# Kernel tuning notes

Hardware: AMD Instinct MI355X
Metric: run time of the kernel (lower is better)

Reference implementation:

```python
import jax, jax.numpy as jnp
import numpy as np

B, C, H, W = 4, 32, 512, 1024  # input feature map
HO, WO = 512, 1024             # output grid


def setup_inputs() -> dict:
    key = jax.random.key(0)
    k1, k2 = jax.random.split(key)
    x = jax.random.normal(k1, (B, C, H, W), dtype=jnp.float32)
    # real-valued (x, y) output coordinates for every input pixel, in-bounds
    scale = jnp.asarray([WO - 1, HO - 1], dtype=jnp.float32)
    sample_map = jax.random.uniform(k2, (H, W, 2), dtype=jnp.float32) * scale
    return {"x": x, "sample_map": sample_map, "out_h": HO, "out_w": WO}


def reference(x, sample_map, out_h, out_w):
    """Bilinear splat: scatter each input pixel x[:,:,i,j] into the output
    at real-valued location sample_map[i,j] = (x_coord, y_coord)."""
    b, c, h, w = x.shape
    n = h * w
    coords = sample_map.reshape(n, 2)
    cx, cy = coords[:, 0], coords[:, 1]
    x0 = jnp.floor(cx)
    y0 = jnp.floor(cy)
    wx = cx - x0  # fractional offsets
    wy = cy - y0
    x0i = x0.astype(jnp.int32)
    y0i = y0.astype(jnp.int32)

    vals = x.reshape(b, c, n)
    out = jnp.zeros((b, c, out_h * out_w), dtype=x.dtype)
    # four bilinear corners: (xi, yi, weight)
    corners = (
        (x0i,     y0i,     (1.0 - wx) * (1.0 - wy)),
        (x0i + 1, y0i,     wx * (1.0 - wy)),
        (x0i,     y0i + 1, (1.0 - wx) * wy),
        (x0i + 1, y0i + 1, wx * wy),
    )
    for xi, yi, wgt in corners:
        valid = (xi >= 0) & (xi < out_w) & (yi >= 0) & (yi < out_h)
        idx = jnp.where(valid, yi * out_w + xi, 0)              # [n]
        wgt = jnp.where(valid, wgt, 0.0).astype(x.dtype)        # [n]
        out = out.at[:, :, idx].add(vals * wgt)
    return out.reshape(b, c, out_h, out_w)
```

## Files before the change

kernel.cpp:

```cpp
#include <hip/hip_runtime.h>

constexpr int Bc   = 4;
constexpr int Cc   = 32;
constexpr int Hc   = 512;
constexpr int Wc   = 1024;
constexpr int HOc  = 512;
constexpr int WOc  = 1024;
constexpr int NPIX  = Hc * Wc;
constexpr int PLANE = HOc * WOc;
constexpr int BCn   = Bc * Cc;

constexpr int TH = 32, TW = 32;
constexpr int TILES_X = WOc / TW;
constexpr int TILES_Y = HOc / TH;
constexpr int NT = TILES_X * TILES_Y;
constexpr int G  = 8;
constexpr int CG = BCn / G;
constexpr int LDSW   = TW + 1;
constexpr int TCELLS = (TH + 1) * (TW + 1);
constexpr int NBIN   = TCELLS + 1;
constexpr int NMAX   = 1280;
constexpr int EMAX   = 4 * NMAX;

__device__ __forceinline__ int tile_of(float cx, float cy, int& x0, int& y0) {
    x0 = (int)floorf(cx);
    y0 = (int)floorf(cy);
    int tx = min(max(x0 >> 5, 0), TILES_X - 1);
    int ty = min(max(y0 >> 5, 0), TILES_Y - 1);
    return ty * TILES_X + tx;
}

__global__ __launch_bounds__(256) void hist_kernel(
    const float2* __restrict__ smap, int* __restrict__ count)
{
    __shared__ int h[NT];
    for (int i = threadIdx.x; i < NT; i += 256) h[i] = 0;
    __syncthreads();
    const int stride = gridDim.x * 256;
    for (int p = blockIdx.x * 256 + threadIdx.x; p < NPIX; p += stride) {
        float2 c = smap[p];
        int x0, y0;
        int t = tile_of(c.x, c.y, x0, y0);
        atomicAdd(&h[t], 1);
    }
    __syncthreads();
    for (int i = threadIdx.x; i < NT; i += 256)
        if (h[i]) atomicAdd(&count[i], h[i]);
}

__global__ __launch_bounds__(512) void scan_kernel(
    const int* __restrict__ count, int* __restrict__ off)
{
    __shared__ int s[NT];
    int tid = threadIdx.x;
    s[tid] = count[tid];
    __syncthreads();
    for (int d = 1; d < NT; d <<= 1) {
        int v = (tid >= d) ? s[tid - d] : 0;
        __syncthreads();
        s[tid] += v;
        __syncthreads();
    }
    if (tid == 0) off[0] = 0;
    off[tid + 1] = s[tid];
}

__global__ __launch_bounds__(256) void scatter_pos_kernel(
    const float2* __restrict__ smap, const int* __restrict__ off,
    int* __restrict__ cursor, int* __restrict__ pos,
    float2* __restrict__ smap_g)
{
    __shared__ int h[NT];
    __shared__ int base[NT];
    const int tid = threadIdx.x;
    for (int i = tid; i < NT; i += 256) h[i] = 0;
    __syncthreads();
    const int p = blockIdx.x * 256 + tid;
    const float2 c = smap[p];
    int x0, y0;
    const int t = tile_of(c.x, c.y, x0, y0);
    atomicAdd(&h[t], 1);
    __syncthreads();
    for (int i = tid; i < NT; i += 256) {
        int cnt = h[i];
        base[i] = cnt ? atomicAdd(&cursor[i], cnt) : 0;
        h[i] = 0;
    }
    __syncthreads();
    const int r = atomicAdd(&h[t], 1);
    const int posi = off[t] + base[t] + r;
    pos[p] = posi;
    smap_g[posi] = c;
}

__global__ __launch_bounds__(256) void cellbuild_kernel(
    const float2* __restrict__ smap_g, const int* __restrict__ off,
    ushort* __restrict__ ent, float* __restrict__ entw,
    int* __restrict__ gcello)
{
    __shared__ unsigned cnt[NBIN];
    __shared__ unsigned coff[NBIN + 1];
    __shared__ unsigned psum[256];
    const int t   = blockIdx.x;
    const int tx0 = (t % TILES_X) * TW;
    const int ty0 = (t / TILES_X) * TH;
    const int lo  = off[t];
    const int n   = off[t + 1] - lo;
    const int nn  = min(n, NMAX);
    const int tid = threadIdx.x;

    for (int i = tid; i < NBIN; i += 256) cnt[i] = 0;
    __syncthreads();

    for (int i = tid; i < nn; i += 256) {
        float2 c = smap_g[lo + i];
        int x0 = (int)floorf(c.x), y0 = (int)floorf(c.y);
        int lx = x0 - tx0, ly = y0 - ty0;
        if ((unsigned)lx < (unsigned)TW && (unsigned)ly < (unsigned)TH) {
            int a = ly * LDSW + lx;
            atomicAdd(&cnt[a], 1u);
            atomicAdd(&cnt[a + 1], 1u);
            atomicAdd(&cnt[a + LDSW], 1u);
            atomicAdd(&cnt[a + LDSW + 1], 1u);
        } else {
            atomicAdd(&cnt[TCELLS], 1u);
        }
    }
    __syncthreads();

    constexpr int BPT = (NBIN + 255) / 256;
    unsigned loc[BPT];
    unsigned s = 0;
    for (int j = 0; j < BPT; ++j) {
        int b = tid * BPT + j;
        unsigned v = (b < NBIN) ? cnt[b] : 0u;
        loc[j] = s; s += v;
    }
    psum[tid] = s;
    __syncthreads();
    for (int d = 1; d < 256; d <<= 1) {
        unsigned v = (tid >= d) ? psum[tid - d] : 0u;
        __syncthreads();
        psum[tid] += v;
        __syncthreads();
    }
    unsigned base = (tid > 0) ? psum[tid - 1] : 0u;
    for (int j = 0; j < BPT; ++j) {
        int b = tid * BPT + j;
        if (b < NBIN) coff[b] = base + loc[j];
    }
    if (tid == 255) coff[NBIN] = psum[255];
    __syncthreads();

    for (int i = tid; i < NBIN; i += 256) cnt[i] = coff[i];
    for (int i = tid; i < NBIN + 1; i += 256)
        gcello[t * (NBIN + 1) + i] = (int)coff[i];
    __syncthreads();

    const int ebase = 4 * lo;
    for (int i = tid; i < nn; i += 256) {
        float2 c = smap_g[lo + i];
        float fx = floorf(c.x), fy = floorf(c.y);
        float wx = c.x - fx, wy = c.y - fy;
        int lx = (int)fx - tx0, ly = (int)fy - ty0;
        if ((unsigned)lx < (unsigned)TW && (unsigned)ly < (unsigned)TH) {
            int a = ly * LDSW + lx;
            float w00 = (1.f - wx) * (1.f - wy), w10 = wx * (1.f - wy);
            float w01 = (1.f - wx) * wy,         w11 = wx * wy;
            unsigned e;
            e = atomicAdd(&cnt[a], 1u);            ent[ebase + e] = (ushort)i; entw[ebase + e] = w00;
            e = atomicAdd(&cnt[a + 1], 1u);        ent[ebase + e] = (ushort)i; entw[ebase + e] = w10;
            e = atomicAdd(&cnt[a + LDSW], 1u);     ent[ebase + e] = (ushort)i; entw[ebase + e] = w01;
            e = atomicAdd(&cnt[a + LDSW + 1], 1u); ent[ebase + e] = (ushort)i; entw[ebase + e] = w11;
        } else {
            unsigned e = atomicAdd(&cnt[TCELLS], 1u);
            ent[ebase + e] = (ushort)i; entw[ebase + e] = 0.f;
        }
    }
}

__global__ __launch_bounds__(256) void gather_kernel(
    const float* __restrict__ x, const int* __restrict__ pos,
    float* __restrict__ xg, int cg0, int ncg)
{
    const int p = (blockIdx.x * 256 + threadIdx.x) * 4;
    const int4 d = *reinterpret_cast<const int4*>(pos + p);
    for (int g = 0; g < ncg; ++g) {
        const float* xp = x + (long)(cg0 + g) * G * NPIX + p;
        float4 r[8];
#pragma unroll
        for (int k = 0; k < 8; ++k)
            r[k] = *reinterpret_cast<const float4*>(xp + (long)k * NPIX);
        float* o0 = xg + ((long)g * NPIX + d.x) * 8;
        float* o1 = xg + ((long)g * NPIX + d.y) * 8;
        float* o2 = xg + ((long)g * NPIX + d.z) * 8;
        float* o3 = xg + ((long)g * NPIX + d.w) * 8;
        *reinterpret_cast<float4*>(o0)     = make_float4(r[0].x, r[1].x, r[2].x, r[3].x);
        *reinterpret_cast<float4*>(o0 + 4) = make_float4(r[4].x, r[5].x, r[6].x, r[7].x);
        *reinterpret_cast<float4*>(o1)     = make_float4(r[0].y, r[1].y, r[2].y, r[3].y);
        *reinterpret_cast<float4*>(o1 + 4) = make_float4(r[4].y, r[5].y, r[6].y, r[7].y);
        *reinterpret_cast<float4*>(o2)     = make_float4(r[0].z, r[1].z, r[2].z, r[3].z);
        *reinterpret_cast<float4*>(o2 + 4) = make_float4(r[4].z, r[5].z, r[6].z, r[7].z);
        *reinterpret_cast<float4*>(o3)     = make_float4(r[0].w, r[1].w, r[2].w, r[3].w);
        *reinterpret_cast<float4*>(o3 + 4) = make_float4(r[4].w, r[5].w, r[6].w, r[7].w);
    }
}

__global__ __launch_bounds__(512) void accum_kernel(
    const float*  __restrict__ xg,
    const float2* __restrict__ smap_g,
    const int*    __restrict__ off,
    const ushort* __restrict__ ent,
    const float*  __restrict__ entw,
    const int*    __restrict__ gcello,
    float*        __restrict__ out, int cg0)
{
    __shared__ float4   vals4[2 * NMAX];
    __shared__ float    wl[EMAX];
    __shared__ unsigned entl[EMAX / 2];
    __shared__ unsigned offl[NBIN + 1];
    const int t     = blockIdx.x;
    const int gslab = blockIdx.y;
    const int bc0   = (cg0 + gslab) * G;
    const int tx0 = (t % TILES_X) * TW;
    const int ty0 = (t / TILES_X) * TH;
    const int tid = threadIdx.x;
    const int lo = off[t], n = off[t + 1] - lo, nn = min(n, NMAX);
    const float* xs = xg + (long)gslab * NPIX * 8;

    const float4* vsrc = (const float4*)(xs + (long)lo * 8);
    for (int j = tid; j < nn * 2; j += 512) vals4[j] = vsrc[j];
    const unsigned* esrc = (const unsigned*)(ent + 4 * lo);
    for (int j = tid; j < nn * 2; j += 512) entl[j] = esrc[j];
    const float* wsrc = entw + 4 * lo;
    for (int j = tid; j < nn * 4; j += 512) wl[j] = wsrc[j];
    for (int j = tid; j < NBIN + 1; j += 512) offl[j] = (unsigned)gcello[t * (NBIN + 1) + j];
    __syncthreads();

    const ushort* entl16 = (const ushort*)entl;

    for (int c = tid; c < TCELLS; c += 512) {
        const unsigned e0 = offl[c], e1 = offl[c + 1];
        float a0 = 0, a1 = 0, a2 = 0, a3 = 0, a4 = 0, a5 = 0, a6 = 0, a7 = 0;
        for (unsigned e = e0; e < e1; ++e) {
            const int idx = entl16[e];
            const float w = wl[e];
            const float4 va = vals4[idx * 2];
            const float4 vb = vals4[idx * 2 + 1];
            a0 += va.x * w; a1 += va.y * w; a2 += va.z * w; a3 += va.w * w;
            a4 += vb.x * w; a5 += vb.y * w; a6 += vb.z * w; a7 += vb.w * w;
        }
        const int r = c / LDSW, cc = c - r * LDSW;
        const int gy = ty0 + r, gx = tx0 + cc;
        if (gy >= HOc || gx >= WOc) continue;
        const bool edge = (r == 0) | (cc == 0) | (r == TH) | (cc == TW);
        const long o = (long)gy * WOc + gx;
        const float av[8] = {a0, a1, a2, a3, a4, a5, a6, a7};
#pragma unroll
        for (int k = 0; k < 8; ++k) {
            float* op = out + (long)(bc0 + k) * PLANE + o;
            if (edge) { if (av[k] != 0.0f) unsafeAtomicAdd(op, av[k]); }
            else      { *op = av[k]; }
        }
    }
    __syncthreads();

    {
        const unsigned e0 = offl[TCELLS], e1 = offl[NBIN];
        for (unsigned e = e0 + tid; e < e1; e += 512) {
            const int idx = entl16[e];
            const float2 c2 = smap_g[lo + idx];
            const float fx = floorf(c2.x), fy = floorf(c2.y);
            const float wx = c2.x - fx, wy = c2.y - fy;
            const int x0 = (int)fx, y0 = (int)fy;
            const float4 va = vals4[idx * 2], vb = vals4[idx * 2 + 1];
            const float v[8] = {va.x, va.y, va.z, va.w, vb.x, vb.y, vb.z, vb.w};
            const float cw[4] = {(1.f - wx) * (1.f - wy), wx * (1.f - wy),
                                 (1.f - wx) * wy,         wx * wy};
            const int cxs[4] = {x0, x0 + 1, x0, x0 + 1};
            const int cys[4] = {y0, y0, y0 + 1, y0 + 1};
#pragma unroll
            for (int q = 0; q < 4; ++q) {
                if (cxs[q] < 0 || cxs[q] >= WOc || cys[q] < 0 || cys[q] >= HOc) continue;
                const long o = (long)cys[q] * WOc + cxs[q];
#pragma unroll
                for (int k = 0; k < 8; ++k)
                    unsafeAtomicAdd(out + (long)(bc0 + k) * PLANE + o, v[k] * cw[q]);
            }
        }
    }

    for (int i = NMAX + tid; i < n; i += 512) {
        const float2 c2 = smap_g[lo + i];
        const float fx = floorf(c2.x), fy = floorf(c2.y);
        const float wx = c2.x - fx, wy = c2.y - fy;
        const int x0 = (int)fx, y0 = (int)fy;
        const float4 va = *((const float4*)(xs + (long)(lo + i) * 8));
        const float4 vb = *((const float4*)(xs + (long)(lo + i) * 8) + 1);
        const float v[8] = {va.x, va.y, va.z, va.w, vb.x, vb.y, vb.z, vb.w};
        const float cw[4] = {(1.f - wx) * (1.f - wy), wx * (1.f - wy),
                             (1.f - wx) * wy,         wx * wy};
        const int cxs[4] = {x0, x0 + 1, x0, x0 + 1};
        const int cys[4] = {y0, y0, y0 + 1, y0 + 1};
#pragma unroll
        for (int q = 0; q < 4; ++q) {
            if (cxs[q] < 0 || cxs[q] >= WOc || cys[q] < 0 || cys[q] >= HOc) continue;
            const long o = (long)cys[q] * WOc + cxs[q];
#pragma unroll
            for (int k = 0; k < 8; ++k)
                unsafeAtomicAdd(out + (long)(bc0 + k) * PLANE + o, v[k] * cw[q]);
        }
    }
}

__global__ __launch_bounds__(256) void splat_kernel(
    const float* __restrict__ x, const float2* __restrict__ smap,
    float* __restrict__ out)
{
    const int p = blockIdx.x * blockDim.x + threadIdx.x;
    if (p >= NPIX) return;
    const float2 c = smap[p];
    const float x0f = floorf(c.x), y0f = floorf(c.y);
    const float wx = c.x - x0f, wy = c.y - y0f;
    const int x0 = (int)x0f, y0 = (int)y0f;
    const float w00 = (1.0f-wx)*(1.0f-wy), w10 = wx*(1.0f-wy);
    const float w01 = (1.0f-wx)*wy, w11 = wx*wy;
    const bool vx0 = (x0>=0)&(x0<WOc), vx1 = (x0+1>=0)&(x0+1<WOc);
    const bool vy0 = (y0>=0)&(y0<HOc), vy1 = (y0+1>=0)&(y0+1<HOc);
    const long base = (long)y0*WOc + x0;
    const int bc0 = blockIdx.y * 4;
#pragma unroll
    for (int k = 0; k < 4; ++k) {
        const int bc = bc0 + k;
        const float v = x[(long)bc*NPIX + p];
        float* o = out + (long)bc*PLANE;
        if (vx0 & vy0) unsafeAtomicAdd(o + base,          v*w00);
        if (vx1 & vy0) unsafeAtomicAdd(o + base + 1,      v*w10);
        if (vx0 & vy1) unsafeAtomicAdd(o + base + WOc,    v*w01);
        if (vx1 & vy1) unsafeAtomicAdd(o + base + WOc+1,  v*w11);
    }
}

extern "C" void kernel_launch(void* const* d_in, const int* in_sizes, int n_in,
                              void* d_out, int out_size, void* d_ws, size_t ws_size,
                              hipStream_t stream) {
    const float*  x    = (const float*)d_in[0];
    const float2* smap = (const float2*)d_in[1];
    float*        out  = (float*)d_out;

    hipMemsetAsync(d_out, 0, (size_t)out_size * sizeof(float), stream);

    const size_t ints = (size_t)NPIX + 3 * NT + 1 + (size_t)NT * (NBIN + 1);
    size_t ofs = (ints * sizeof(int) + 255) & ~(size_t)255;
    const size_t smapg_ofs = ofs;
    ofs += sizeof(float2) * (size_t)NPIX;
    ofs = (ofs + 255) & ~(size_t)255;
    const size_t ent_ofs = ofs;
    ofs += sizeof(ushort) * 4 * (size_t)NPIX;
    ofs = (ofs + 255) & ~(size_t)255;
    const size_t entw_ofs = ofs;
    ofs += sizeof(float) * 4 * (size_t)NPIX;
    ofs = (ofs + 255) & ~(size_t)255;
    const size_t xg_ofs = ofs;
    const size_t slab_bytes = (size_t)NPIX * G * sizeof(float);

    long slabs = 0;
    if (ws_size > xg_ofs) slabs = (long)((ws_size - xg_ofs) / slab_bytes);
    if (slabs > CG) slabs = CG;

    if (slabs < 1) {
        dim3 grid(NPIX / 256, BCn / 4);
        splat_kernel<<<grid, 256, 0, stream>>>(x, smap, out);
        return;
    }

    char* wsb      = (char*)d_ws;
    int*  pos      = (int*)wsb;
    int*  count    = pos + NPIX;
    int*  cursor   = count + NT;
    int*  off      = cursor + NT;
    int*  gcello   = off + NT + 1;
    float2* smap_g = (float2*)(wsb + smapg_ofs);
    ushort* ent    = (ushort*)(wsb + ent_ofs);
    float*  entw   = (float*)(wsb + entw_ofs);
    float*  xg     = (float*)(wsb + xg_ofs);

    hipMemsetAsync(count, 0, sizeof(int) * 2 * NT, stream);

    hist_kernel       <<<256, 256, 0, stream>>>(smap, count);
    scan_kernel       <<<1, 512, 0, stream>>>(count, off);
    scatter_pos_kernel<<<NPIX / 256, 256, 0, stream>>>(smap, off, cursor, pos, smap_g);
    cellbuild_kernel  <<<NT, 256, 0, stream>>>(smap_g, off, ent, entw, gcello);

    for (int cg0 = 0; cg0 < CG; cg0 += (int)slabs) {
        int ncg = CG - cg0;
        if (ncg > slabs) ncg = (int)slabs;
        gather_kernel<<<NPIX / 1024, 256, 0, stream>>>(x, pos, xg, cg0, ncg);
        dim3 grid2(NT, ncg);
        accum_kernel <<<grid2, 512, 0, stream>>>(xg, smap_g, off, ent, entw, gcello, out, cg0);
    }
}
```

Before: 1.981 ms.

## Drop LDS staging in accum kernel, read gathered values directly from global

The accumulation kernel no longer stages per-tile values, entry indices and weights into shared memory. It reads them straight from global memory, and the cache is expected to serve the reuse. The gathered layout widens to 16 channels per pixel, and each slab is split across two blocks of 8 channels. Both blocks of a pair touch the same pixel rows, which should improve cache locality. This removes the shared-memory footprint and the barriers, so occupancy can rise, but each entry now costs uncached-at-first global loads.

```diff
diff --git a/kernel.cpp b/kernel.cpp
--- a/kernel.cpp
+++ b/kernel.cpp
@@ -14,13 +14,12 @@
 constexpr int TILES_X = WOc / TW;
 constexpr int TILES_Y = HOc / TH;
 constexpr int NT = TILES_X * TILES_Y;
-constexpr int G  = 8;
-constexpr int CG = BCn / G;
+constexpr int CH16 = 16;
+constexpr int CG16 = BCn / CH16;
 constexpr int LDSW   = TW + 1;
 constexpr int TCELLS = (TH + 1) * (TW + 1);
 constexpr int NBIN   = TCELLS + 1;
 constexpr int NMAX   = 1280;
-constexpr int EMAX   = 4 * NMAX;
 
 __device__ __forceinline__ int tile_of(float cx, float cy, int& x0, int& y0) {
     x0 = (int)floorf(cx);
@@ -181,72 +180,61 @@
 
 __global__ __launch_bounds__(256) void gather_kernel(
     const float* __restrict__ x, const int* __restrict__ pos,
-    float* __restrict__ xg, int cg0, int ncg)
-{
-    const int p = (blockIdx.x * 256 + threadIdx.x) * 4;
-    const int4 d = *reinterpret_cast<const int4*>(pos + p);
-    for (int g = 0; g < ncg; ++g) {
-        const float* xp = x + (long)(cg0 + g) * G * NPIX + p;
-        float4 r[8];
-#pragma unroll
-        for (int k = 0; k < 8; ++k)
-            r[k] = *reinterpret_cast<const float4*>(xp + (long)k * NPIX);
-        float* o0 = xg + ((long)g * NPIX + d.x) * 8;
-        float* o1 = xg + ((long)g * NPIX + d.y) * 8;
-        float* o2 = xg + ((long)g * NPIX + d.z) * 8;
-        float* o3 = xg + ((long)g * NPIX + d.w) * 8;
-        *reinterpret_cast<float4*>(o0)     = make_float4(r[0].x, r[1].x, r[2].x, r[3].x);
-        *reinterpret_cast<float4*>(o0 + 4) = make_float4(r[4].x, r[5].x, r[6].x, r[7].x);
-        *reinterpret_cast<float4*>(o1)     = make_float4(r[0].y, r[1].y, r[2].y, r[3].y);
-        *reinterpret_cast<float4*>(o1 + 4) = make_float4(r[4].y, r[5].y, r[6].y, r[7].y);
-        *reinterpret_cast<float4*>(o2)     = make_float4(r[0].z, r[1].z, r[2].z, r[3].z);
-        *reinterpret_cast<float4*>(o2 + 4) = make_float4(r[4].z, r[5].z, r[6].z, r[7].z);
-        *reinterpret_cast<float4*>(o3)     = make_float4(r[0].w, r[1].w, r[2].w, r[3].w);
-        *reinterpret_cast<float4*>(o3 + 4) = make_float4(r[4].w, r[5].w, r[6].w, r[7].w);
-    }
-}
-
-__global__ __launch_bounds__(512) void accum_kernel(
+    float* __restrict__ xg, int cg016, int ncg16)
+{
+    const int p = (blockIdx.x * 256 + threadIdx.x) * 2;
+    const int2 d = *reinterpret_cast<const int2*>(pos + p);
+    for (int g = 0; g < ncg16; ++g) {
+        const float* xp = x + (long)(cg016 + g) * CH16 * NPIX + p;
+        float2 r[16];
+#pragma unroll
+        for (int k = 0; k < 16; ++k)
+            r[k] = *reinterpret_cast<const float2*>(xp + (long)k * NPIX);
+        float* o0 = xg + ((long)g * NPIX + d.x) * 16;
+        float* o1 = xg + ((long)g * NPIX + d.y) * 16;
+        *reinterpret_cast<float4*>(o0)      = make_float4(r[0].x,  r[1].x,  r[2].x,  r[3].x);
+        *reinterpret_cast<float4*>(o0 + 4)  = make_float4(r[4].x,  r[5].x,  r[6].x,  r[7].x);
+        *reinterpret_cast<float4*>(o0 + 8)  = make_float4(r[8].x,  r[9].x,  r[10].x, r[11].x);
+        *reinterpret_cast<float4*>(o0 + 12) = make_float4(r[12].x, r[13].x, r[14].x, r[15].x);
+        *reinterpret_cast<float4*>(o1)      = make_float4(r[0].y,  r[1].y,  r[2].y,  r[3].y);
+        *reinterpret_cast<float4*>(o1 + 4)  = make_float4(r[4].y,  r[5].y,  r[6].y,  r[7].y);
+        *reinterpret_cast<float4*>(o1 + 8)  = make_float4(r[8].y,  r[9].y,  r[10].y, r[11].y);
+        *reinterpret_cast<float4*>(o1 + 12) = make_float4(r[12].y, r[13].y, r[14].y, r[15].y);
+    }
+}
+
+__global__ __launch_bounds__(256) void accum_kernel(
     const float*  __restrict__ xg,
     const float2* __restrict__ smap_g,
     const int*    __restrict__ off,
     const ushort* __restrict__ ent,
     const float*  __restrict__ entw,
     const int*    __restrict__ gcello,
-    float*        __restrict__ out, int cg0)
-{
-    __shared__ float4   vals4[2 * NMAX];
-    __shared__ float    wl[EMAX];
-    __shared__ unsigned entl[EMAX / 2];
-    __shared__ unsigned offl[NBIN + 1];
-    const int t     = blockIdx.x;
-    const int gslab = blockIdx.y;
-    const int bc0   = (cg0 + gslab) * G;
+    float*        __restrict__ out, int cg016)
+{
+    const int t    = blockIdx.x;
+    const int yb   = blockIdx.y;
+    const int s16  = yb >> 1;
+    const int half = yb & 1;
+    const int bc0  = (cg016 + s16) * CH16 + half * 8;
     const int tx0 = (t % TILES_X) * TW;
     const int ty0 = (t / TILES_X) * TH;
     const int tid = threadIdx.x;
-    const int lo = off[t], n = off[t + 1] - lo, nn = min(n, NMAX);
-    const float* xs = xg + (long)gslab * NPIX * 8;
-
-    const float4* vsrc = (const float4*)(xs + (long)lo * 8);
-    for (int j = tid; j < nn * 2; j += 512) vals4[j] = vsrc[j];
-    const unsigned* esrc = (const unsigned*)(ent + 4 * lo);
-    for (int j = tid; j < nn * 2; j += 512) entl[j] = esrc[j];
-    const float* wsrc = entw + 4 * lo;
-    for (int j = tid; j < nn * 4; j += 512) wl[j] = wsrc[j];
-    for (int j = tid; j < NBIN + 1; j += 512) offl[j] = (unsigned)gcello[t * (NBIN + 1) + j];
-    __syncthreads();
-
-    const ushort* entl16 = (const ushort*)entl;
-
-    for (int c = tid; c < TCELLS; c += 512) {
-        const unsigned e0 = offl[c], e1 = offl[c + 1];
+    const int lo = off[t], n = off[t + 1] - lo;
+    const float*  xs = xg + ((long)s16 * NPIX + lo) * 16 + half * 8;
+    const ushort* ep = ent  + 4 * (long)lo;
+    const float*  wp = entw + 4 * (long)lo;
+    const int*    go = gcello + t * (NBIN + 1);
+
+    for (int c = tid; c < TCELLS; c += 256) {
+        const int e0 = go[c], e1 = go[c + 1];
         float a0 = 0, a1 = 0, a2 = 0, a3 = 0, a4 = 0, a5 = 0, a6 = 0, a7 = 0;
-        for (unsigned e = e0; e < e1; ++e) {
-            const int idx = entl16[e];
-            const float w = wl[e];
-            const float4 va = vals4[idx * 2];
-            const float4 vb = vals4[idx * 2 + 1];
+        for (int e = e0; e < e1; ++e) {
+            const int idx = ep[e];
+            const float w = wp[e];
+            const float* vp = xs + (long)idx * 16;
+            const float4 va = *reinterpret_cast<const float4*>(vp);
+            const float4 vb = *reinterpret_cast<const float4*>(vp + 4);
             a0 += va.x * w; a1 += va.y * w; a2 += va.z * w; a3 += va.w * w;
             a4 += vb.x * w; a5 += vb.y * w; a6 += vb.z * w; a7 += vb.w * w;
         }
@@ -263,17 +251,18 @@
             else      { *op = av[k]; }
         }
     }
-    __syncthreads();
 
     {
-        const unsigned e0 = offl[TCELLS], e1 = offl[NBIN];
-        for (unsigned e = e0 + tid; e < e1; e += 512) {
-            const int idx = entl16[e];
+        const int e0 = go[TCELLS], e1 = go[NBIN];
+        for (int e = e0 + tid; e < e1; e += 256) {
+            const int idx = ep[e];
             const float2 c2 = smap_g[lo + idx];
             const float fx = floorf(c2.x), fy = floorf(c2.y);
             const float wx = c2.x - fx, wy = c2.y - fy;
             const int x0 = (int)fx, y0 = (int)fy;
-            const float4 va = vals4[idx * 2], vb = vals4[idx * 2 + 1];
+            const float* vp = xs + (long)idx * 16;
+            const float4 va = *reinterpret_cast<const float4*>(vp);
+            const float4 vb = *reinterpret_cast<const float4*>(vp + 4);
             const float v[8] = {va.x, va.y, va.z, va.w, vb.x, vb.y, vb.z, vb.w};
             const float cw[4] = {(1.f - wx) * (1.f - wy), wx * (1.f - wy),
                                  (1.f - wx) * wy,         wx * wy};
@@ -290,13 +279,14 @@
         }
     }
 
-    for (int i = NMAX + tid; i < n; i += 512) {
+    for (int i = NMAX + tid; i < n; i += 256) {
         const float2 c2 = smap_g[lo + i];
         const float fx = floorf(c2.x), fy = floorf(c2.y);
         const float wx = c2.x - fx, wy = c2.y - fy;
         const int x0 = (int)fx, y0 = (int)fy;
-        const float4 va = *((const float4*)(xs + (long)(lo + i) * 8));
-        const float4 vb = *((const float4*)(xs + (long)(lo + i) * 8) + 1);
+        const float* vp = xs + (long)i * 16;
+        const float4 va = *reinterpret_cast<const float4*>(vp);
+        const float4 vb = *reinterpret_cast<const float4*>(vp + 4);
         const float v[8] = {va.x, va.y, va.z, va.w, vb.x, vb.y, vb.z, vb.w};
         const float cw[4] = {(1.f - wx) * (1.f - wy), wx * (1.f - wy),
                              (1.f - wx) * wy,         wx * wy};
@@ -362,11 +352,11 @@
     ofs += sizeof(float) * 4 * (size_t)NPIX;
     ofs = (ofs + 255) & ~(size_t)255;
     const size_t xg_ofs = ofs;
-    const size_t slab_bytes = (size_t)NPIX * G * sizeof(float);
+    const size_t slab_bytes = (size_t)NPIX * CH16 * sizeof(float);
 
     long slabs = 0;
     if (ws_size > xg_ofs) slabs = (long)((ws_size - xg_ofs) / slab_bytes);
-    if (slabs > CG) slabs = CG;
+    if (slabs > CG16) slabs = CG16;
 
     if (slabs < 1) {
         dim3 grid(NPIX / 256, BCn / 4);
@@ -392,11 +382,11 @@
     scatter_pos_kernel<<<NPIX / 256, 256, 0, stream>>>(smap, off, cursor, pos, smap_g);
     cellbuild_kernel  <<<NT, 256, 0, stream>>>(smap_g, off, ent, entw, gcello);
 
-    for (int cg0 = 0; cg0 < CG; cg0 += (int)slabs) {
-        int ncg = CG - cg0;
+    for (int cg016 = 0; cg016 < CG16; cg016 += (int)slabs) {
+        int ncg = CG16 - cg016;
         if (ncg > slabs) ncg = (int)slabs;
-        gather_kernel<<<NPIX / 1024, 256, 0, stream>>>(x, pos, xg, cg0, ncg);
-        dim3 grid2(NT, ncg);
-        accum_kernel <<<grid2, 512, 0, stream>>>(xg, smap_g, off, ent, entw, gcello, out, cg0);
-    }
-}
+        gather_kernel<<<NPIX / 512, 256, 0, stream>>>(x, pos, xg, cg016, ncg);
+        dim3 grid2(NT, ncg * 2);
+        accum_kernel <<<grid2, 256, 0, stream>>>(xg, smap_g, off, ent, entw, gcello, out, cg016);
+    }
+}
```

After: 2.663 ms. 34.4% more time.
